# Performance work log

Hardware: AMD Instinct MI355X
Metric: run time of the kernel (lower is better)

Reference implementation:

```python
import jax, jax.numpy as jnp
import numpy as np
jax.config.update("jax_enable_x64", True)  # int64 hash codes for lattice keys

N_KPTS = 32768
C = 61      # feature channels; f-MLP input dim is C+3 = 64
D = 64      # disp-distribution channels
D_LAT = 8   # last f-layer output -> permutohedral position dim

# large odd 62-bit multipliers for the lattice-key hash (wraps mod 2^64)
_MULTS = np.array([2654435761405764093, 1181783497276652981,
                   3202034522624059733, 2685821657736338717,
                   1876998521354586173, 1481765933965188213,
                   2549297995355413921, 3373259426345127233], dtype=np.int64)


def _hcode(k, mults):
    return jnp.sum(k.astype(jnp.int64) * mults, axis=-1)


def _pl_filter(pos, vals):
    """Permutohedral lattice splat -> blur -> slice (approx. Gaussian filter).
    pos: (N, d) float32 lattice positions, vals: (N, vd) float32 values."""
    N, d = pos.shape
    vd = vals.shape[1]
    M = N * (d + 1)  # fixed-size hash table (every point touches d+1 vertices)
    # --- elevate onto hyperplane H_d in R^{d+1} ---
    scale = np.float32(np.sqrt(2.0 / 3.0) * (d + 1)) / np.sqrt(
        np.arange(1, d + 1, dtype=np.float32) * np.arange(2, d + 2, dtype=np.float32))
    E = np.zeros((d + 1, d), dtype=np.float32)
    E[0, :] = 1.0
    for i in range(1, d + 1):
        E[i, i - 1] = -float(i)
        E[i, i:] = 1.0
    elevated = (pos * jnp.asarray(scale, jnp.float32)) @ jnp.asarray(E).T  # (N, d+1)
    # --- nearest zero-colored lattice point and simplex ranks ---
    rem0 = jnp.floor(elevated / (d + 1) + 0.5) * (d + 1)
    sum_val = jnp.round(jnp.sum(rem0, -1) / (d + 1)).astype(jnp.int32)
    diff = elevated - rem0
    rank = jnp.argsort(jnp.argsort(-diff, axis=-1), axis=-1).astype(jnp.int32) + sum_val[:, None]
    lo = rank < 0
    hi = rank > d
    rem0 = rem0 + jnp.where(lo, float(d + 1), 0.0) - jnp.where(hi, float(d + 1), 0.0)
    rank = rank + jnp.where(lo, d + 1, 0) - jnp.where(hi, d + 1, 0)
    # --- barycentric coordinates ---
    t = (elevated - rem0) / (d + 1)
    rows = jnp.arange(N)[:, None]
    bary = jnp.zeros((N, d + 2), jnp.float32)
    bary = bary.at[rows, d - rank].add(t)
    bary = bary.at[rows, d + 1 - rank].add(-t)
    bary = bary.at[:, 0].add(1.0 + bary[:, d + 1])
    w = bary[:, :d + 1]  # (N, d+1) vertex weights
    # --- simplex vertex keys (first d coords; full key sums to 0) ---
    canonical = np.zeros((d + 1, d + 1), np.int32)
    for r in range(d + 1):
        canonical[r, :d + 1 - r] = r
        canonical[r, d + 1 - r:] = r - (d + 1)
    keys = rem0.astype(jnp.int32)[None, :, :d] + jnp.asarray(canonical)[:, rank[:, :d]]  # (d+1,N,d)
    # --- hash table via sorted unique codes (jit-safe fixed size) ---
    mults = jnp.asarray(_MULTS[:d])
    codes = _hcode(keys, mults).reshape(M)
    uniq, inv = jnp.unique(codes, return_inverse=True, size=M,
                           fill_value=jnp.iinfo(jnp.int64).max)
    inv = inv.reshape(M)
    # --- splat ---
    wv = (w.T[:, :, None] * vals[None]).reshape(M, vd)
    lat = jax.ops.segment_sum(wv, inv, num_segments=M)  # (M, vd)
    occ = jax.ops.segment_sum(jnp.ones((M,), jnp.float32), inv, num_segments=M) > 0
    ukeys = jnp.zeros((M, d), jnp.int32).at[inv].set(keys.reshape(M, d))
    # --- blur along each of the d+1 lattice directions ---
    for j in range(d + 1):
        off = np.ones(d + 1, np.int32)
        off[j] = -d
        o = jnp.asarray(off[:d])
        def _nbr(sign, lat=lat):
            c = _hcode(ukeys + sign * o, mults)
            i = jnp.clip(jnp.searchsorted(uniq, c), 0, M - 1)
            ok = (jnp.take(uniq, i) == c) & jnp.take(occ, i)
            return jnp.where(ok[:, None], jnp.take(lat, i, axis=0), 0.0)
        lat = jnp.where(occ[:, None], 0.5 * lat + 0.25 * (_nbr(1) + _nbr(-1)), lat)
    # --- slice ---
    alpha = 1.0 / (1.0 + 2.0 ** (-d))
    return jnp.sum(w.T[:, :, None] * jnp.take(lat, inv, axis=0).reshape(d + 1, N, vd), 0) * alpha


def _layernorm2(x, g, b):
    # LayerNorm(normalized_shape=(N, K)): stats over the last TWO dims jointly
    mu = jnp.mean(x, axis=(-2, -1), keepdims=True)
    var = jnp.mean((x - mu) ** 2, axis=(-2, -1), keepdims=True)
    return (x - mu) * jax.lax.rsqrt(var + 1e-5) * g + b


def setup_inputs() -> dict:
    key = jax.random.key(0)
    ks = jax.random.split(key, 16)
    f32 = jnp.float32
    rn = lambda k, shape, s=1.0: jax.random.normal(k, shape, dtype=f32) * s
    inp = {
        "kpts": rn(ks[0], (1, N_KPTS, 3)),
        "disps_distr": rn(ks[1], (1, N_KPTS, D)),
        "feats": rn(ks[2], (1, N_KPTS, C)),
    }
    i = 3
    for b in range(2):
        inp[f"Wd{b}0"] = rn(ks[i], (D, D), 0.05); i += 1
        inp[f"bd{b}0"] = jnp.zeros((D,), f32)
        inp[f"Wd{b}1"] = rn(ks[i], (D, D), 0.05); i += 1
        inp[f"bd{b}1"] = jnp.zeros((D,), f32)
        inp[f"Wf{b}"] = rn(ks[i], (C + 3, D_LAT), 0.1); i += 1
        inp[f"bf{b}"] = jnp.zeros((D_LAT,), f32)
        inp[f"g{b}"] = jnp.ones((N_KPTS, D_LAT), f32)
        inp[f"be{b}"] = jnp.zeros((N_KPTS, D_LAT), f32)
    return inp


def reference(kpts, disps_distr, feats, Wd00, bd00, Wd01, bd01, Wf0, bf0, g0, be0,
              Wd10, bd10, Wd11, bd11, Wf1, bf1, g1, be1):
    fk = jnp.concatenate([kpts, feats], axis=-1)  # (1, N, C+3)
    x = jnp.reshape(disps_distr, (1, N_KPTS, -1))
    blocks = [(Wd00, bd00, Wd01, bd01, Wf0, bf0, g0, be0),
              (Wd10, bd10, Wd11, bd11, Wf1, bf1, g1, be1)]
    for (Wd0, bd0, Wd1, bd1, Wf, bf, g, be) in blocks:
        x = jax.nn.relu(x @ Wd0 + bd0)   # d-layer 0
        x = jax.nn.relu(x @ Wd1 + bd1)   # d-layer 1
        # only the LAST f-layer output is used by the torch code (feats_kpts is never updated)
        pos = _layernorm2(jax.nn.relu(fk @ Wf + bf), g, be)  # (1, N, 8)
        x = _pl_filter(pos[0], x[0])[None]
    return x
```

## Files before the change

kernel.cpp:

```cpp
#include <hip/hip_runtime.h>
#include <hip/hip_bf16.h>
#include <hip/hip_fp16.h>
#include <stdint.h>

typedef unsigned long long u64;

#define NK 32768
#define DL 8
#define DP1 9
#define MT (NK*DP1)
#define HBITS 19
#define HSIZE (1u<<HBITS)
#define HMASK (HSIZE-1)
#define EMPTY_CODE 0xFFFFFFFFFFFFFFFFULL
#define NBLK 1152
#define HBLK (HSIZE/256)
#define CAP 32
#define MAXHUB 16384

#define MLPB (NK/16)
#define POSB (NK/32)
#define EMBB (NK/256)
#define HZB  384
#define VZB  128
#define NBRB (9*MT/256)
#define SPAB (MT/8)
#define SPBB 1152

__device__ __constant__ u64 c_mults[8] = {
    2654435761405764093ULL, 1181783497276652981ULL, 3202034522624059733ULL,
    2685821657736338717ULL, 1876998521354586173ULL, 1481765933965188213ULL,
    2549297995355413921ULL, 3373259426345127233ULL};

__device__ __forceinline__ unsigned int hmix(u64 x) {
    return (unsigned int)(x >> (64 - HBITS)) & HMASK;
}

__device__ __forceinline__ u64 dir_delta(int j) {
    u64 s = 0;
    #pragma unroll
    for (int k = 0; k < 8; k++) s += c_mults[k];
    return (j == 8) ? s : (s - 9ULL * c_mults[j]);
}

__device__ __forceinline__ float ldf(const void* p, int i, int bf) {
    if (bf) return __bfloat162float(((const __hip_bfloat16*)p)[i]);
    return ((const float*)p)[i];
}

__global__ void k_detect(const unsigned* __restrict__ g0w, int* __restrict__ flag,
                         double* __restrict__ stats) {
    if (threadIdx.x == 0) {
        int f = 1;
        for (int i = 0; i < 8; i++) if (g0w[i] != 0x3F803F80u) f = 0;
        *flag = f;
        stats[0] = 0.0; stats[1] = 0.0;
    }
}

__global__ __launch_bounds__(256) void k_mlppos(const void* __restrict__ xin, int use_df_in,
    const void* __restrict__ W0, const void* __restrict__ B0,
    const void* __restrict__ W1, const void* __restrict__ B1,
    float* __restrict__ xout, const int* __restrict__ df,
    const void* __restrict__ kpts, const void* __restrict__ feats,
    const void* __restrict__ Wf, const void* __restrict__ Bf,
    float* __restrict__ pos_pre, double* __restrict__ stats) {
    __shared__ union {
        struct { float w0[4096], w1[4096], xs[16][64], y1[16][64]; } m;
        struct { float wf[512]; float fk[32][65]; float red[256], red2[256]; } p;
    } sm;
    int bf = *df;
    int tid = threadIdx.x;
    if (blockIdx.x < MLPB) {
        int bfin = use_df_in ? bf : 0;
        int row0 = blockIdx.x * 16;
        for (int i = tid; i < 4096; i += 256) { sm.m.w0[i] = ldf(W0, i, bf); sm.m.w1[i] = ldf(W1, i, bf); }
        for (int i = tid; i < 1024; i += 256) sm.m.xs[i>>6][i&63] = ldf(xin, row0*64 + i, bfin);
        __syncthreads();
        int rb = tid >> 6, col = tid & 63;
        float b0c = ldf(B0, col, bf);
        float a0 = b0c, a1 = b0c, a2 = b0c, a3 = b0c;
        #pragma unroll
        for (int k = 0; k < 64; k++) {
            float w = sm.m.w0[k*64+col];
            a0 = fmaf(sm.m.xs[rb   ][k], w, a0);
            a1 = fmaf(sm.m.xs[rb+ 4][k], w, a1);
            a2 = fmaf(sm.m.xs[rb+ 8][k], w, a2);
            a3 = fmaf(sm.m.xs[rb+12][k], w, a3);
        }
        sm.m.y1[rb   ][col] = fmaxf(a0, 0.f);
        sm.m.y1[rb+ 4][col] = fmaxf(a1, 0.f);
        sm.m.y1[rb+ 8][col] = fmaxf(a2, 0.f);
        sm.m.y1[rb+12][col] = fmaxf(a3, 0.f);
        __syncthreads();
        float b1c = ldf(B1, col, bf);
        a0 = b1c; a1 = b1c; a2 = b1c; a3 = b1c;
        #pragma unroll
        for (int k = 0; k < 64; k++) {
            float w = sm.m.w1[k*64+col];
            a0 = fmaf(sm.m.y1[rb   ][k], w, a0);
            a1 = fmaf(sm.m.y1[rb+ 4][k], w, a1);
            a2 = fmaf(sm.m.y1[rb+ 8][k], w, a2);
            a3 = fmaf(sm.m.y1[rb+12][k], w, a3);
        }
        xout[(row0+rb   )*64 + col] = fmaxf(a0, 0.f);
        xout[(row0+rb+ 4)*64 + col] = fmaxf(a1, 0.f);
        xout[(row0+rb+ 8)*64 + col] = fmaxf(a2, 0.f);
        xout[(row0+rb+12)*64 + col] = fmaxf(a3, 0.f);
    } else {
        int n0 = (blockIdx.x - MLPB) * 32;
        for (int i = tid; i < 512; i += 256) sm.p.wf[i] = ldf(Wf, i, bf);
        for (int i = tid; i < 32*64; i += 256) {
            int pt = i >> 6, k = i & 63, n = n0 + pt;
            sm.p.fk[pt][k] = (k < 3) ? ldf(kpts, n*3 + k, bf) : ldf(feats, n*61 + (k-3), bf);
        }
        __syncthreads();
        int pt = tid >> 3, j = tid & 7, n = n0 + pt;
        float acc = ldf(Bf, j, bf);
        #pragma unroll
        for (int k = 0; k < 64; k++) acc = fmaf(sm.p.fk[pt][k], sm.p.wf[k*8+j], acc);
        acc = fmaxf(acc, 0.f);
        pos_pre[n*8 + j] = acc;
        sm.p.red[tid] = acc; sm.p.red2[tid] = acc * acc;
        __syncthreads();
        for (int s = 128; s > 0; s >>= 1) {
            if (tid < s) { sm.p.red[tid] += sm.p.red[tid+s]; sm.p.red2[tid] += sm.p.red2[tid+s]; }
            __syncthreads();
        }
        if (tid == 0) { atomicAdd(&stats[0], (double)sm.p.red[0]); atomicAdd(&stats[1], (double)sm.p.red2[0]); }
    }
}

__global__ __launch_bounds__(256) void k_embedz(const float* __restrict__ pos_pre,
    const double* __restrict__ stats, const void* __restrict__ g,
    const void* __restrict__ be, float* __restrict__ wgt,
    u64* __restrict__ pcodes, int* __restrict__ cnt, int* __restrict__ cnt2,
    int* __restrict__ hubid, const int* __restrict__ df,
    u64* __restrict__ htabc, float* __restrict__ hubval) {
    int bid = blockIdx.x;
    if (bid >= EMBB) {
        if (bid < EMBB + HZB) {
            uint4 f; f.x = 0xFFFFFFFFu; f.y = 0xFFFFFFFFu; f.z = 0xFFFFFFFFu; f.w = 0xFFFFFFFFu;
            for (int i = (bid - EMBB) * 256 + threadIdx.x; i < (int)(HSIZE/2); i += HZB * 256)
                ((uint4*)htabc)[i] = f;
        } else {
            uint4 z; z.x = 0; z.y = 0; z.z = 0; z.w = 0;
            for (int i = (bid - EMBB - HZB) * 256 + threadIdx.x; i < MAXHUB*16; i += VZB * 256)
                ((uint4*)hubval)[i] = z;
        }
        return;
    }
    int bf = *df;
    int n = bid * 256 + threadIdx.x;
    if (n >= NK) return;
    const double inv_cnt = 1.0 / (double)(NK * DL);
    double mud = stats[0] * inv_cnt;
    double vard = stats[1] * inv_cnt - mud * mud;
    float mu = (float)mud;
    float rs = rsqrtf((float)vard + 1e-5f);
    const float scale[8] = {
        5.196152422706632f, 3.0f, 2.1213203435596424f, 1.643167672515498f,
        1.3416407864998738f, 1.1338934190276817f, 0.9819805060619657f, 0.8660254037844386f};
    float c[8];
    #pragma unroll
    for (int k = 0; k < 8; k++) {
        float v = pos_pre[n*8 + k];
        float p = (v - mu) * rs * ldf(g, n*8 + k, bf) + ldf(be, n*8 + k, bf);
        c[k] = p * scale[k];
    }
    float sufa[9]; sufa[8] = 0.f;
    #pragma unroll
    for (int k = 7; k >= 0; k--) sufa[k] = sufa[k+1] + c[k];
    float elev[9];
    elev[0] = sufa[0];
    #pragma unroll
    for (int i = 1; i < 9; i++) elev[i] = sufa[i] - (float)i * c[i-1];
    int ri[9], sumv = 0;
    float diff[9];
    #pragma unroll
    for (int i = 0; i < 9; i++) {
        ri[i] = (int)floorf(elev[i] / 9.0f + 0.5f);
        sumv += ri[i];
        diff[i] = elev[i] - 9.f * (float)ri[i];
    }
    int rank[9];
    #pragma unroll
    for (int i = 0; i < 9; i++) {
        int r = 0;
        #pragma unroll
        for (int j = 0; j < 9; j++)
            r += (diff[j] > diff[i]) || ((diff[j] == diff[i]) && (j < i));
        rank[i] = r + sumv;
    }
    #pragma unroll
    for (int i = 0; i < 9; i++) {
        if (rank[i] < 0)      { rank[i] += 9; ri[i] += 1; }
        else if (rank[i] > 8) { rank[i] -= 9; ri[i] -= 1; }
    }
    float t[9];
    #pragma unroll
    for (int i = 0; i < 9; i++) t[i] = (elev[i] - 9.f * (float)ri[i]) / 9.f;
    float bary[10];
    #pragma unroll
    for (int i = 0; i < 10; i++) bary[i] = 0.f;
    #pragma unroll
    for (int i = 0; i < 9; i++) { bary[8 - rank[i]] += t[i]; bary[9 - rank[i]] -= t[i]; }
    bary[0] += 1.f + bary[9];
    for (int r = 0; r < 9; r++) {
        u64 code = 0;
        #pragma unroll
        for (int k = 0; k < 8; k++) {
            int key = 9 * ri[k] + ((rank[k] <= 8 - r) ? r : (r - 9));
            code += (u64)(long long)key * c_mults[k];
        }
        int m = n * 9 + r;
        wgt[m] = bary[r];
        pcodes[m] = code;
        cnt[m] = 0;
        cnt2[m] = 0;
        hubid[m] = -1;
    }
}

__global__ __launch_bounds__(256) void k_insert(const u64* __restrict__ pcodes,
    u64* __restrict__ htab_code, unsigned int* __restrict__ ppos) {
    int m = blockIdx.x * 256 + threadIdx.x;
    if (m >= MT) return;
    u64 code = pcodes[m];
    unsigned int pos = hmix(code);
    for (;;) {
        u64 cc = htab_code[pos];
        if (cc == code) break;
        if (cc == EMPTY_CODE) {
            u64 old = atomicCAS(&htab_code[pos], EMPTY_CODE, code);
            if (old == EMPTY_CODE || old == code) break;
        }
        pos = (pos + 1) & HMASK;
    }
    ppos[m] = pos;
}

__global__ __launch_bounds__(256) void k_occ(const u64* __restrict__ htab_code,
    int* __restrict__ bocc) {
    __shared__ int wcnt[4];
    unsigned int i = blockIdx.x * 256 + threadIdx.x;
    bool occ = (htab_code[i] != EMPTY_CODE);
    u64 mask = __ballot(occ);
    int lane = threadIdx.x & 63;
    if (lane == 0) wcnt[threadIdx.x >> 6] = __popcll(mask);
    __syncthreads();
    if (threadIdx.x == 0) bocc[blockIdx.x] = wcnt[0] + wcnt[1] + wcnt[2] + wcnt[3];
}

__global__ __launch_bounds__(256) void k_occscan(int* __restrict__ bocc,
    int* __restrict__ counter, int* __restrict__ nhub) {
    __shared__ int s[256];
    __shared__ int carry;
    int t = threadIdx.x;
    if (t == 0) { carry = 0; *nhub = 0; }
    __syncthreads();
    for (int c = 0; c < HBLK / 256; c++) {
        int i = c * 256 + t;
        int v = bocc[i];
        s[t] = v; __syncthreads();
        for (int off = 1; off < 256; off <<= 1) {
            int a = (t >= off) ? s[t-off] : 0;
            __syncthreads();
            s[t] += a;
            __syncthreads();
        }
        int cl = carry;
        bocc[i] = s[t] - v + cl;
        __syncthreads();
        if (t == 0) carry = cl + s[255];
        __syncthreads();
    }
    if (t == 0) *counter = carry;
}

__global__ __launch_bounds__(256) void k_assign2(const u64* __restrict__ htab_code,
    const int* __restrict__ bocc, int* __restrict__ htab_slot,
    u64* __restrict__ slot_code) {
    __shared__ int wbase[4];
    unsigned int i = blockIdx.x * 256 + threadIdx.x;
    u64 cde = htab_code[i];
    bool occ = (cde != EMPTY_CODE);
    int lane = threadIdx.x & 63;
    int wid  = threadIdx.x >> 6;
    u64 mask = __ballot(occ);
    int prefix = __popcll(mask & ((1ULL << lane) - 1ULL));
    if (lane == 0) wbase[wid] = __popcll(mask);
    __syncthreads();
    if (threadIdx.x == 0) {
        int run = bocc[blockIdx.x];
        for (int w = 0; w < 4; w++) { int c = wbase[w]; wbase[w] = run; run += c; }
    }
    __syncthreads();
    if (occ) {
        int s = wbase[wid] + prefix;
        htab_slot[i] = s;
        slot_code[s] = cde;
    }
}

__global__ __launch_bounds__(256) void k_nbrlookup(const u64* __restrict__ slot_code,
    const u64* __restrict__ htab_code, const int* __restrict__ htab_slot,
    const int* __restrict__ counter, int2* __restrict__ nbr,
    const unsigned int* __restrict__ ppos, int* __restrict__ sidx,
    int* __restrict__ cnt) {
    if (blockIdx.x < NBRB) {
        int idx = blockIdx.x * 256 + threadIdx.x;
        int j = idx / MT;
        int sl = idx - j * MT;
        int count = *counter;
        if (sl >= count) return;
        u64 dj = dir_delta(j);
        u64 code = slot_code[sl];
        int res[2];
        #pragma unroll
        for (int s = 0; s < 2; s++) {
            u64 cde = code + (s ? (u64)(0ULL - dj) : dj);
            unsigned int pos = hmix(cde);
            int r = -1;
            for (;;) {
                u64 cc = htab_code[pos];
                if (cc == cde) { r = htab_slot[pos]; break; }
                if (cc == EMPTY_CODE) break;
                pos = (pos + 1) & HMASK;
            }
            res[s] = r;
        }
        nbr[j * MT + sl] = make_int2(res[0], res[1]);
    } else {
        int m = (blockIdx.x - NBRB) * 256 + threadIdx.x;
        if (m >= MT) return;
        int s = htab_slot[ppos[m]];
        sidx[m] = s;
        atomicAdd(&cnt[s], 1);
    }
}

__global__ __launch_bounds__(256) void k_scan1(const int* __restrict__ cnt,
    int* __restrict__ exbuf, int* __restrict__ bsum,
    int* __restrict__ hublist, int* __restrict__ hubid, int* __restrict__ nhub) {
    __shared__ int s[256];
    int t = threadIdx.x;
    int i = blockIdx.x * 256 + t;
    int v = cnt[i];
    if (v > CAP) {
        int h = atomicAdd(nhub, 1);
        if (h < MAXHUB) { hublist[h] = i; hubid[i] = h; }
    }
    s[t] = v; __syncthreads();
    for (int off = 1; off < 256; off <<= 1) {
        int a = (t >= off) ? s[t-off] : 0;
        __syncthreads();
        s[t] += a;
        __syncthreads();
    }
    exbuf[i] = s[t] - v;
    if (t == 255) bsum[blockIdx.x] = s[255];
}

__global__ __launch_bounds__(256) void k_scan2(int* __restrict__ bsum) {
    __shared__ int s[256];
    __shared__ int carry;
    int t = threadIdx.x;
    if (t == 0) carry = 0;
    __syncthreads();
    for (int c = 0; c < (NBLK + 255) / 256; c++) {
        int i = c * 256 + t;
        int v = (i < NBLK) ? bsum[i] : 0;
        s[t] = v; __syncthreads();
        for (int off = 1; off < 256; off <<= 1) {
            int a = (t >= off) ? s[t-off] : 0;
            __syncthreads();
            s[t] += a;
            __syncthreads();
        }
        int cl = carry;
        if (i < NBLK) bsum[i] = s[t] - v + cl;
        __syncthreads();
        if (t == 0) carry = cl + s[255];
        __syncthreads();
    }
}

__global__ __launch_bounds__(256) void k_scatter(const int* __restrict__ sidx,
    const int* __restrict__ exbuf, const int* __restrict__ bsum,
    int* __restrict__ cnt2, int* __restrict__ list) {
    int m = blockIdx.x * 256 + threadIdx.x;
    if (m < MT) {
        int s = sidx[m];
        int ofs = atomicAdd(&cnt2[s], 1);
        list[exbuf[s] + bsum[s >> 8] + ofs] = m;
    }
}

__global__ __launch_bounds__(256) void k_splat(const float* __restrict__ xbuf,
    const float* __restrict__ wgt, const int* __restrict__ exbuf,
    const int* __restrict__ bsum, const int* __restrict__ cnt,
    const int* __restrict__ list, __half* __restrict__ val,
    const int* __restrict__ counter, const int* __restrict__ sidx,
    const int* __restrict__ hubid, float* __restrict__ hubval) {
    const float2* x2 = (const float2*)xbuf;
    int lane = threadIdx.x & 31;
    if (blockIdx.x < SPAB) {
        int count = *counter;
        int sl = blockIdx.x * 8 + (threadIdx.x >> 5);
        if (sl >= count) return;
        int c = cnt[sl];
        if (c > CAP) return;
        int st = exbuf[sl] + bsum[sl >> 8];
        float2 acc = make_float2(0.f, 0.f);
        int mm = 0; float ww = 0.f;
        if (lane < c) { mm = list[st + lane]; ww = wgt[mm]; }
        for (int k = 0; k < c; k++) {
            int   m = __shfl(mm, k, 32);
            float w = __shfl(ww, k, 32);
            float2 xv = x2[(m / 9) * 32 + lane];
            acc.x = fmaf(w, xv.x, acc.x);
            acc.y = fmaf(w, xv.y, acc.y);
        }
        ((__half2*)val)[(size_t)sl * 32 + lane] = __float22half2_rn(acc);
    } else {
        int chunk = (blockIdx.x - SPAB) * 8 + (threadIdx.x >> 5);
        int e = chunk * 32 + lane;
        int m = 0, hid = -1; float w = 0.f; int hub = 0;
        if (e < MT) {
            m = list[e];
            int slot = sidx[m];
            hub = (cnt[slot] > CAP);
            if (hub) { w = wgt[m]; hid = hubid[slot]; }
        }
        u64 bal = __ballot(hub);
        unsigned int half = (threadIdx.x & 32) ? (unsigned int)(bal >> 32) : (unsigned int)bal;
        if (!half) return;
        float2 acc = make_float2(0.f, 0.f);
        int cur = -1;
        while (half) {
            int k = __ffs(half) - 1; half &= half - 1;
            int   hk = __shfl(hid, k, 32);
            int   mk = __shfl(m, k, 32);
            float wk = __shfl(w, k, 32);
            float2 xv = x2[(mk / 9) * 32 + lane];
            if (hk != cur) {
                if (cur >= 0) {
                    atomicAdd(&hubval[(size_t)cur * 64 + 2*lane    ], acc.x);
                    atomicAdd(&hubval[(size_t)cur * 64 + 2*lane + 1], acc.y);
                }
                cur = hk; acc = make_float2(0.f, 0.f);
            }
            acc.x = fmaf(wk, xv.x, acc.x);
            acc.y = fmaf(wk, xv.y, acc.y);
        }
        atomicAdd(&hubval[(size_t)cur * 64 + 2*lane    ], acc.x);
        atomicAdd(&hubval[(size_t)cur * 64 + 2*lane + 1], acc.y);
    }
}

__global__ __launch_bounds__(256) void k_hubcvt(const float* __restrict__ hubval,
    const int* __restrict__ hublist, const int* __restrict__ nhub,
    __half* __restrict__ val) {
    int idx = blockIdx.x * 256 + threadIdx.x;
    int hi = idx >> 5, lane = idx & 31;
    if (hi >= *nhub) return;
    int sl = hublist[hi];
    float2 v = ((const float2*)hubval)[(size_t)hi * 32 + lane];
    ((__half2*)val)[(size_t)sl * 32 + lane] = __float22half2_rn(v);
}

__global__ __launch_bounds__(256) void k_blur(const __half* __restrict__ vin,
    __half* __restrict__ vout, const int2* __restrict__ nbrj,
    const int* __restrict__ counter) {
    int idx = blockIdx.x * 256 + threadIdx.x;
    int sl = idx >> 3, lane = idx & 7;
    int count = *counter;
    if (sl >= count) return;
    int2 nbp = nbrj[sl];
    typedef union { uint4 u; __half2 h[4]; } row16;
    const uint4* vin4 = (const uint4*)vin;
    uint4* vout4 = (uint4*)vout;
    row16 S, A, B, O;
    S.u = vin4[(size_t)sl*8 + lane];
    uint4 z; z.x = 0; z.y = 0; z.z = 0; z.w = 0;
    A.u = (nbp.x >= 0) ? vin4[(size_t)nbp.x*8 + lane] : z;
    B.u = (nbp.y >= 0) ? vin4[(size_t)nbp.y*8 + lane] : z;
    #pragma unroll
    for (int k = 0; k < 4; k++) {
        float2 fs = __half22float2(S.h[k]);
        float2 fa = __half22float2(A.h[k]);
        float2 fb = __half22float2(B.h[k]);
        float2 r;
        r.x = 0.5f * fs.x + 0.25f * (fa.x + fb.x);
        r.y = 0.5f * fs.y + 0.25f * (fa.y + fb.y);
        O.h[k] = __float22half2_rn(r);
    }
    vout4[(size_t)sl*8 + lane] = O.u;
}

__global__ __launch_bounds__(256) void k_slice(const float* __restrict__ wgt,
    const int* __restrict__ sidx, const __half* __restrict__ val,
    float* __restrict__ outf, void* __restrict__ outb, int write_out,
    const int* __restrict__ df, double* __restrict__ stats) {
    int idx = blockIdx.x * 256 + threadIdx.x;
    if (idx == 0) { stats[0] = 0.0; stats[1] = 0.0; }
    if (idx >= NK * 32) return;
    int bf = *df;
    const __half2* v2 = (const __half2*)val;
    int n = idx >> 5, cp = idx & 31;
    float2 acc = make_float2(0.f, 0.f);
    #pragma unroll
    for (int r = 0; r < 9; r++) {
        int m = n * 9 + r;
        float w = wgt[m];
        float2 hv = __half22float2(v2[(size_t)sidx[m]*32 + cp]);
        acc.x = fmaf(w, hv.x, acc.x);
        acc.y = fmaf(w, hv.y, acc.y);
    }
    acc.x *= 0.9961089494163424f;
    acc.y *= 0.9961089494163424f;
    int o = n*64 + cp*2;
    if (write_out) {
        if (bf) {
            __hip_bfloat16* ob = (__hip_bfloat16*)outb;
            ob[o]   = __float2bfloat16(acc.x);
            ob[o+1] = __float2bfloat16(acc.y);
        } else {
            float* of = (float*)outb;
            of[o] = acc.x; of[o+1] = acc.y;
        }
    } else {
        outf[o] = acc.x; outf[o+1] = acc.y;
    }
}

extern "C" void kernel_launch(void* const* d_in, const int* in_sizes, int n_in,
                              void* d_out, int out_size, void* d_ws, size_t ws_size,
                              hipStream_t stream) {
    const void* kpts  = d_in[0];
    const void* disps = d_in[1];
    const void* feats = d_in[2];

    char* p = (char*)d_ws;
    float* xbuf     = (float*)p;  p += (size_t)NK*64*4;
    float* pos_pre  = (float*)p;  p += (size_t)NK*8*4;
    double* stats   = (double*)p; p += 256;
    int*   dflag    = (int*)p;    p += 256;
    float* wgt      = (float*)p;  p += (size_t)MT*4;
    int*   sidx     = (int*)p;    p += (size_t)MT*4;
    u64*   pcodes   = (u64*)p;    p += (size_t)MT*8;
    unsigned int* ppos = (unsigned int*)p; p += (size_t)MT*4;
    u64*   htabc    = (u64*)p;    p += (size_t)HSIZE*8;
    int*   htabs    = (int*)p;    p += (size_t)HSIZE*4;
    u64*   slotc    = (u64*)p;    p += (size_t)MT*8;
    int*   counter  = (int*)p;    p += 256;
    int*   nhub     = (int*)p;    p += 256;
    int*   bocc     = (int*)p;    p += (size_t)HBLK*4;
    int*   cnt      = (int*)p;    p += (size_t)MT*4;
    int*   cnt2     = (int*)p;    p += (size_t)MT*4;
    int*   hubid    = (int*)p;    p += (size_t)MT*4;
    int*   exbuf    = (int*)p;    p += (size_t)MT*4;
    int*   list     = (int*)p;    p += (size_t)MT*4;
    int*   bsum     = (int*)p;    p += 256*32;
    int*   hublist  = (int*)p;    p += (size_t)MAXHUB*4;
    float* hubval   = (float*)p;  p += (size_t)MAXHUB*64*4;
    int2*  nbr      = (int2*)p;   p += (size_t)MT*9*8;
    __half* valA    = (__half*)p; p += (size_t)MT*64*2;
    __half* valB    = (__half*)p; p += (size_t)MT*64*2;

    k_detect<<<1, 64, 0, stream>>>((const unsigned*)d_in[3 + 6], dflag, stats);

    for (int b = 0; b < 2; b++) {
        const void* W0 = d_in[3 + b*8 + 0];
        const void* B0 = d_in[3 + b*8 + 1];
        const void* W1 = d_in[3 + b*8 + 2];
        const void* B1 = d_in[3 + b*8 + 3];
        const void* Wf = d_in[3 + b*8 + 4];
        const void* Bf = d_in[3 + b*8 + 5];
        const void* G  = d_in[3 + b*8 + 6];
        const void* Be = d_in[3 + b*8 + 7];

        k_mlppos<<<MLPB + POSB, 256, 0, stream>>>(
            b == 0 ? disps : (const void*)xbuf, b == 0 ? 1 : 0,
            W0, B0, W1, B1, xbuf, dflag,
            kpts, feats, Wf, Bf, pos_pre, stats);

        k_embedz<<<EMBB + HZB + VZB, 256, 0, stream>>>(pos_pre, stats, G, Be, wgt,
                                                       pcodes, cnt, cnt2, hubid, dflag,
                                                       htabc, hubval);
        k_insert<<<NBLK, 256, 0, stream>>>(pcodes, htabc, ppos);
        k_occ<<<HBLK, 256, 0, stream>>>(htabc, bocc);
        k_occscan<<<1, 256, 0, stream>>>(bocc, counter, nhub);
        k_assign2<<<HBLK, 256, 0, stream>>>(htabc, bocc, htabs, slotc);
        k_nbrlookup<<<NBRB + NBLK, 256, 0, stream>>>(slotc, htabc, htabs, counter, nbr,
                                                     ppos, sidx, cnt);

        k_scan1<<<NBLK, 256, 0, stream>>>(cnt, exbuf, bsum, hublist, hubid, nhub);
        k_scan2<<<1, 256, 0, stream>>>(bsum);
        k_scatter<<<NBLK, 256, 0, stream>>>(sidx, exbuf, bsum, cnt2, list);
        k_splat<<<SPAB + SPBB, 256, 0, stream>>>(xbuf, wgt, exbuf, bsum, cnt, list,
                                                 valA, counter, sidx, hubid, hubval);
        k_hubcvt<<<(MAXHUB*32)/256, 256, 0, stream>>>(hubval, hublist, nhub, valA);

        for (int j = 0; j < 9; j++) {
            const __half* vin = (j & 1) ? valB : valA;
            __half*       vout = (j & 1) ? valA : valB;
            k_blur<<<(MT*8 + 255)/256, 256, 0, stream>>>(vin, vout, nbr + (size_t)j*MT, counter);
        }
        k_slice<<<(NK*64)/256, 256, 0, stream>>>(wgt, sidx, valB, xbuf,
                                                 d_out, b == 1 ? 1 : 0, dflag, stats);
    }
}
```

Measured before the change: 733.6 us.

## Amortize MLP weight staging across four row tiles with transposed padded weights

The MLP part of the fused kernel now runs 512 blocks, each processing four 16-row tiles, so the 64x64 weight matrices are loaded into shared memory once per four tiles instead of once per tile. Weights are stored transposed with a padded stride so each thread reads its column as float4 vectors, and inputs are loaded with vectorized float4/ushort4 loads. This cuts redundant global weight traffic and LDS instruction count, at the cost of fewer blocks (less parallelism) and an extra sync per tile.

```diff
diff --git a/kernel.cpp b/kernel.cpp
--- a/kernel.cpp
+++ b/kernel.cpp
@@ -18,7 +18,7 @@
 #define CAP 32
 #define MAXHUB 16384
 
-#define MLPB (NK/16)
+#define MLPB 512
 #define POSB (NK/32)
 #define EMBB (NK/256)
 #define HZB  384
@@ -26,6 +26,7 @@
 #define NBRB (9*MT/256)
 #define SPAB (MT/8)
 #define SPBB 1152
+#define WP 68
 
 __device__ __constant__ u64 c_mults[8] = {
     2654435761405764093ULL, 1181783497276652981ULL, 3202034522624059733ULL,
@@ -46,6 +47,20 @@
 __device__ __forceinline__ float ldf(const void* p, int i, int bf) {
     if (bf) return __bfloat162float(((const __hip_bfloat16*)p)[i]);
     return ((const float*)p)[i];
+}
+
+__device__ __forceinline__ float bf2f(unsigned short u) {
+    union { unsigned u; float f; } c; c.u = ((unsigned)u) << 16; return c.f;
+}
+
+__device__ __forceinline__ float4 ld4(const void* p, int vi, int bf) {
+    if (bf) {
+        ushort4 u = ((const ushort4*)p)[vi];
+        float4 r;
+        r.x = bf2f(u.x); r.y = bf2f(u.y); r.z = bf2f(u.z); r.w = bf2f(u.w);
+        return r;
+    }
+    return ((const float4*)p)[vi];
 }
 
 __global__ void k_detect(const unsigned* __restrict__ g0w, int* __restrict__ flag,
@@ -66,47 +81,76 @@
     const void* __restrict__ Wf, const void* __restrict__ Bf,
     float* __restrict__ pos_pre, double* __restrict__ stats) {
     __shared__ union {
-        struct { float w0[4096], w1[4096], xs[16][64], y1[16][64]; } m;
+        struct { float w0t[64*WP], w1t[64*WP], xs[16][64], y1[16][64]; } m;
         struct { float wf[512]; float fk[32][65]; float red[256], red2[256]; } p;
     } sm;
     int bf = *df;
     int tid = threadIdx.x;
     if (blockIdx.x < MLPB) {
         int bfin = use_df_in ? bf : 0;
-        int row0 = blockIdx.x * 16;
-        for (int i = tid; i < 4096; i += 256) { sm.m.w0[i] = ldf(W0, i, bf); sm.m.w1[i] = ldf(W1, i, bf); }
-        for (int i = tid; i < 1024; i += 256) sm.m.xs[i>>6][i&63] = ldf(xin, row0*64 + i, bfin);
-        __syncthreads();
+        for (int i = tid; i < 1024; i += 256) {
+            float4 v0 = ld4(W0, i, bf);
+            float4 v1 = ld4(W1, i, bf);
+            int k = i >> 4, c0 = (i & 15) * 4;
+            sm.m.w0t[(c0+0)*WP + k] = v0.x; sm.m.w0t[(c0+1)*WP + k] = v0.y;
+            sm.m.w0t[(c0+2)*WP + k] = v0.z; sm.m.w0t[(c0+3)*WP + k] = v0.w;
+            sm.m.w1t[(c0+0)*WP + k] = v1.x; sm.m.w1t[(c0+1)*WP + k] = v1.y;
+            sm.m.w1t[(c0+2)*WP + k] = v1.z; sm.m.w1t[(c0+3)*WP + k] = v1.w;
+        }
         int rb = tid >> 6, col = tid & 63;
         float b0c = ldf(B0, col, bf);
-        float a0 = b0c, a1 = b0c, a2 = b0c, a3 = b0c;
-        #pragma unroll
-        for (int k = 0; k < 64; k++) {
-            float w = sm.m.w0[k*64+col];
-            a0 = fmaf(sm.m.xs[rb   ][k], w, a0);
-            a1 = fmaf(sm.m.xs[rb+ 4][k], w, a1);
-            a2 = fmaf(sm.m.xs[rb+ 8][k], w, a2);
-            a3 = fmaf(sm.m.xs[rb+12][k], w, a3);
-        }
-        sm.m.y1[rb   ][col] = fmaxf(a0, 0.f);
-        sm.m.y1[rb+ 4][col] = fmaxf(a1, 0.f);
-        sm.m.y1[rb+ 8][col] = fmaxf(a2, 0.f);
-        sm.m.y1[rb+12][col] = fmaxf(a3, 0.f);
-        __syncthreads();
         float b1c = ldf(B1, col, bf);
-        a0 = b1c; a1 = b1c; a2 = b1c; a3 = b1c;
-        #pragma unroll
-        for (int k = 0; k < 64; k++) {
-            float w = sm.m.w1[k*64+col];
-            a0 = fmaf(sm.m.y1[rb   ][k], w, a0);
-            a1 = fmaf(sm.m.y1[rb+ 4][k], w, a1);
-            a2 = fmaf(sm.m.y1[rb+ 8][k], w, a2);
-            a3 = fmaf(sm.m.y1[rb+12][k], w, a3);
-        }
-        xout[(row0+rb   )*64 + col] = fmaxf(a0, 0.f);
-        xout[(row0+rb+ 4)*64 + col] = fmaxf(a1, 0.f);
-        xout[(row0+rb+ 8)*64 + col] = fmaxf(a2, 0.f);
-        xout[(row0+rb+12)*64 + col] = fmaxf(a3, 0.f);
+        const float4* wc0 = (const float4*)&sm.m.w0t[col*WP];
+        const float4* wc1 = (const float4*)&sm.m.w1t[col*WP];
+        for (int t = 0; t < 4; t++) {
+            int row0 = (blockIdx.x * 4 + t) * 16;
+            __syncthreads();
+            *(float4*)&sm.m.xs[tid>>4][(tid&15)*4] = ld4(xin, row0*16 + tid, bfin);
+            __syncthreads();
+            float a0 = b0c, a1 = b0c, a2 = b0c, a3 = b0c;
+            #pragma unroll
+            for (int kk = 0; kk < 16; kk++) {
+                float4 w  = wc0[kk];
+                float4 x0 = *(const float4*)&sm.m.xs[rb   ][kk*4];
+                float4 x1 = *(const float4*)&sm.m.xs[rb+ 4][kk*4];
+                float4 x2 = *(const float4*)&sm.m.xs[rb+ 8][kk*4];
+                float4 x3 = *(const float4*)&sm.m.xs[rb+12][kk*4];
+                a0 = fmaf(x0.x, w.x, a0); a0 = fmaf(x0.y, w.y, a0);
+                a0 = fmaf(x0.z, w.z, a0); a0 = fmaf(x0.w, w.w, a0);
+                a1 = fmaf(x1.x, w.x, a1); a1 = fmaf(x1.y, w.y, a1);
+                a1 = fmaf(x1.z, w.z, a1); a1 = fmaf(x1.w, w.w, a1);
+                a2 = fmaf(x2.x, w.x, a2); a2 = fmaf(x2.y, w.y, a2);
+                a2 = fmaf(x2.z, w.z, a2); a2 = fmaf(x2.w, w.w, a2);
+                a3 = fmaf(x3.x, w.x, a3); a3 = fmaf(x3.y, w.y, a3);
+                a3 = fmaf(x3.z, w.z, a3); a3 = fmaf(x3.w, w.w, a3);
+            }
+            sm.m.y1[rb   ][col] = fmaxf(a0, 0.f);
+            sm.m.y1[rb+ 4][col] = fmaxf(a1, 0.f);
+            sm.m.y1[rb+ 8][col] = fmaxf(a2, 0.f);
+            sm.m.y1[rb+12][col] = fmaxf(a3, 0.f);
+            __syncthreads();
+            a0 = b1c; a1 = b1c; a2 = b1c; a3 = b1c;
+            #pragma unroll
+            for (int kk = 0; kk < 16; kk++) {
+                float4 w  = wc1[kk];
+                float4 x0 = *(const float4*)&sm.m.y1[rb   ][kk*4];
+                float4 x1 = *(const float4*)&sm.m.y1[rb+ 4][kk*4];
+                float4 x2 = *(const float4*)&sm.m.y1[rb+ 8][kk*4];
+                float4 x3 = *(const float4*)&sm.m.y1[rb+12][kk*4];
+                a0 = fmaf(x0.x, w.x, a0); a0 = fmaf(x0.y, w.y, a0);
+                a0 = fmaf(x0.z, w.z, a0); a0 = fmaf(x0.w, w.w, a0);
+                a1 = fmaf(x1.x, w.x, a1); a1 = fmaf(x1.y, w.y, a1);
+                a1 = fmaf(x1.z, w.z, a1); a1 = fmaf(x1.w, w.w, a1);
+                a2 = fmaf(x2.x, w.x, a2); a2 = fmaf(x2.y, w.y, a2);
+                a2 = fmaf(x2.z, w.z, a2); a2 = fmaf(x2.w, w.w, a2);
+                a3 = fmaf(x3.x, w.x, a3); a3 = fmaf(x3.y, w.y, a3);
+                a3 = fmaf(x3.z, w.z, a3); a3 = fmaf(x3.w, w.w, a3);
+            }
+            xout[(row0+rb   )*64 + col] = fmaxf(a0, 0.f);
+            xout[(row0+rb+ 4)*64 + col] = fmaxf(a1, 0.f);
+            xout[(row0+rb+ 8)*64 + col] = fmaxf(a2, 0.f);
+            xout[(row0+rb+12)*64 + col] = fmaxf(a3, 0.f);
+        }
     } else {
         int n0 = (blockIdx.x - MLPB) * 32;
         for (int i = tid; i < 512; i += 256) sm.p.wf[i] = ldf(Wf, i, bf);
```

Result: slower. 819.6 us (+11.7%).

## Rework MLP blocks to keep rows in registers and broadcast via readlane

Applied to the files above, without the earlier changes.

The two-layer d-MLP part of the fused kernel now handles 64 rows per block instead of 16, cutting the block count and the repeated staging of the 32 KB weight tiles into shared memory. Weights are loaded with vectorized float4/bf16x4 loads. Each wavefront keeps 8 input rows in registers, one element per lane, and broadcasts the k-th element with readlane, so the input and hidden tiles no longer go through shared memory and the intermediate barrier is gone. In exchange there are more registers per thread, one readlane per FMA, and fewer blocks to overlap with the position branch.

```diff
diff --git a/kernel.cpp b/kernel.cpp
--- a/kernel.cpp
+++ b/kernel.cpp
@@ -18,7 +18,7 @@
 #define CAP 32
 #define MAXHUB 16384
 
-#define MLPB (NK/16)
+#define MLPB 512
 #define POSB (NK/32)
 #define EMBB (NK/256)
 #define HZB  384
@@ -46,6 +46,24 @@
 __device__ __forceinline__ float ldf(const void* p, int i, int bf) {
     if (bf) return __bfloat162float(((const __hip_bfloat16*)p)[i]);
     return ((const float*)p)[i];
+}
+
+__device__ __forceinline__ float bf2f(unsigned short u) {
+    union { unsigned u; float f; } c; c.u = ((unsigned)u) << 16; return c.f;
+}
+
+__device__ __forceinline__ float4 ld4(const void* p, int vi, int bf) {
+    if (bf) {
+        ushort4 u = ((const ushort4*)p)[vi];
+        float4 r;
+        r.x = bf2f(u.x); r.y = bf2f(u.y); r.z = bf2f(u.z); r.w = bf2f(u.w);
+        return r;
+    }
+    return ((const float4*)p)[vi];
+}
+
+__device__ __forceinline__ float rdlane(float v, int k) {
+    return __uint_as_float(__builtin_amdgcn_readlane(__float_as_uint(v), k));
 }
 
 __global__ void k_detect(const unsigned* __restrict__ g0w, int* __restrict__ flag,
@@ -66,47 +84,49 @@
     const void* __restrict__ Wf, const void* __restrict__ Bf,
     float* __restrict__ pos_pre, double* __restrict__ stats) {
     __shared__ union {
-        struct { float w0[4096], w1[4096], xs[16][64], y1[16][64]; } m;
+        struct { float w0[4096], w1[4096]; } m;
         struct { float wf[512]; float fk[32][65]; float red[256], red2[256]; } p;
     } sm;
     int bf = *df;
     int tid = threadIdx.x;
     if (blockIdx.x < MLPB) {
         int bfin = use_df_in ? bf : 0;
-        int row0 = blockIdx.x * 16;
-        for (int i = tid; i < 4096; i += 256) { sm.m.w0[i] = ldf(W0, i, bf); sm.m.w1[i] = ldf(W1, i, bf); }
-        for (int i = tid; i < 1024; i += 256) sm.m.xs[i>>6][i&63] = ldf(xin, row0*64 + i, bfin);
-        __syncthreads();
-        int rb = tid >> 6, col = tid & 63;
-        float b0c = ldf(B0, col, bf);
-        float a0 = b0c, a1 = b0c, a2 = b0c, a3 = b0c;
-        #pragma unroll
-        for (int k = 0; k < 64; k++) {
-            float w = sm.m.w0[k*64+col];
-            a0 = fmaf(sm.m.xs[rb   ][k], w, a0);
-            a1 = fmaf(sm.m.xs[rb+ 4][k], w, a1);
-            a2 = fmaf(sm.m.xs[rb+ 8][k], w, a2);
-            a3 = fmaf(sm.m.xs[rb+12][k], w, a3);
-        }
-        sm.m.y1[rb   ][col] = fmaxf(a0, 0.f);
-        sm.m.y1[rb+ 4][col] = fmaxf(a1, 0.f);
-        sm.m.y1[rb+ 8][col] = fmaxf(a2, 0.f);
-        sm.m.y1[rb+12][col] = fmaxf(a3, 0.f);
-        __syncthreads();
-        float b1c = ldf(B1, col, bf);
-        a0 = b1c; a1 = b1c; a2 = b1c; a3 = b1c;
-        #pragma unroll
-        for (int k = 0; k < 64; k++) {
-            float w = sm.m.w1[k*64+col];
-            a0 = fmaf(sm.m.y1[rb   ][k], w, a0);
-            a1 = fmaf(sm.m.y1[rb+ 4][k], w, a1);
-            a2 = fmaf(sm.m.y1[rb+ 8][k], w, a2);
-            a3 = fmaf(sm.m.y1[rb+12][k], w, a3);
-        }
-        xout[(row0+rb   )*64 + col] = fmaxf(a0, 0.f);
-        xout[(row0+rb+ 4)*64 + col] = fmaxf(a1, 0.f);
-        xout[(row0+rb+ 8)*64 + col] = fmaxf(a2, 0.f);
-        xout[(row0+rb+12)*64 + col] = fmaxf(a3, 0.f);
+        for (int i = tid; i < 1024; i += 256) {
+            ((float4*)sm.m.w0)[i] = ld4(W0, i, bf);
+            ((float4*)sm.m.w1)[i] = ld4(W1, i, bf);
+        }
+        __syncthreads();
+        int lane = tid & 63, wv = tid >> 6;
+        float b0c = ldf(B0, lane, bf);
+        float b1c = ldf(B1, lane, bf);
+        for (int t = 0; t < 2; t++) {
+            int row0 = (blockIdx.x * 2 + t) * 32 + wv * 8;
+            float a[8], acc[8];
+            #pragma unroll
+            for (int r = 0; r < 8; r++) {
+                a[r] = ldf(xin, (row0 + r) * 64 + lane, bfin);
+                acc[r] = b0c;
+            }
+            #pragma unroll 8
+            for (int k = 0; k < 64; k++) {
+                float w = sm.m.w0[k * 64 + lane];
+                #pragma unroll
+                for (int r = 0; r < 8; r++)
+                    acc[r] = fmaf(rdlane(a[r], k), w, acc[r]);
+            }
+            #pragma unroll
+            for (int r = 0; r < 8; r++) { a[r] = fmaxf(acc[r], 0.f); acc[r] = b1c; }
+            #pragma unroll 8
+            for (int k = 0; k < 64; k++) {
+                float w = sm.m.w1[k * 64 + lane];
+                #pragma unroll
+                for (int r = 0; r < 8; r++)
+                    acc[r] = fmaf(rdlane(a[r], k), w, acc[r]);
+            }
+            #pragma unroll
+            for (int r = 0; r < 8; r++)
+                xout[(row0 + r) * 64 + lane] = fmaxf(acc[r], 0.f);
+        }
     } else {
         int n0 = (blockIdx.x - MLPB) * 32;
         for (int i = tid; i < 512; i += 256) sm.p.wf[i] = ldf(Wf, i, bf);
```

Measured after the change: 710.4 us. 1.03x faster.
